# Performance work log

Measured on AMD Instinct MI355X. Metric: run time of the kernel, lower is better.

Reference implementation:

```python
import jax, jax.numpy as jnp
import numpy as np
import math

G, T, D, B = 20000, 1536, 512, 256
TOPK = 32


def setup_inputs() -> dict:
    key = jax.random.key(0)
    k1, k2, k3, k4 = jax.random.split(key, 4)
    tg_dec = jax.random.normal(k1, (G, D), dtype=jnp.float32)
    tf_base = jax.random.normal(k2, (T, D), dtype=jnp.float32)
    tf_expr = jax.random.normal(k3, (B, T), dtype=jnp.float32)
    motif_mask = jax.random.randint(k4, (G, T), 0, 2).astype(jnp.int32)
    scale = jnp.full((1,), 0.1, dtype=jnp.float32)  # nn.Parameter scale
    return {"tg_dec": tg_dec, "tf_base": tf_base, "tf_expr": tf_expr,
            "motif_mask": motif_mask, "scale": scale}


def reference(tg_dec, tf_base, tf_expr, motif_mask, scale):
    # scaled similarity: [G, T]
    sim = jnp.matmul(tg_dec, tf_base.T) / math.sqrt(tf_base.shape[1])
    # masked fill where motif prior is absent
    sim = jnp.where(motif_mask == 0, -jnp.inf, sim)
    attn = jax.nn.softmax(sim, axis=-1)
    attn = jnp.nan_to_num(attn, nan=0.0)
    # top-k selection + scatter mask + renormalize
    _, topk_idx = jax.lax.top_k(attn, TOPK)              # [G, TOPK]
    rows = jnp.arange(attn.shape[0])[:, None]
    mask = jnp.zeros_like(attn).at[rows, topk_idx].set(1.0)
    attn = attn * mask
    attn = attn / (attn.sum(axis=-1, keepdims=True) + 1e-8)
    # weighted combine: [B, G]
    tf_scalar = jnp.matmul(tf_expr, attn.T)
    # dropout is identity in eval mode
    return (scale[0] * tf_scalar, attn)
```

## Files before the change

kernel.cpp:

```cpp
#include <hip/hip_runtime.h>
#include <cstdint>

typedef unsigned short u16;
typedef unsigned int   u32;
typedef unsigned long long u64;

#define G_ROWS 20000
#define G_PAD  20096
#define T_DIM  1536
#define D_DIM  512
#define B_DIM  256
#define TOPK   32
#define SIM_SCALE 0.04419417382415922f
#define SQRT_D    22.62741699796952f
#define BOUND_EPS 2.0e-4f

typedef __bf16 bf16x8 __attribute__((ext_vector_type(8)));
typedef float  f32x4  __attribute__((ext_vector_type(4)));

__device__ __forceinline__ u16 f2bf(float f) {
  u32 u = __float_as_uint(f);
  u += 0x7fffu + ((u >> 16) & 1u);
  return (u16)(u >> 16);
}
__device__ __forceinline__ float bf2f(u16 h) {
  return __uint_as_float(((u32)h) << 16);
}
__device__ __forceinline__ u32 fkey(float v) {
  u32 b = __float_as_uint(v);
  return (b & 0x80000000u) ? ~b : (b | 0x80000000u);
}
__device__ __forceinline__ float funkey(u32 o) {
  u32 b = (o & 0x80000000u) ? (o & 0x7FFFFFFFu) : ~o;
  return __uint_as_float(b);
}

__global__ __launch_bounds__(256) void prep(const float* __restrict__ tg_dec,
                                            const float* __restrict__ tf_base,
                                            const float* __restrict__ tf_expr,
                                            u16* __restrict__ Ah, u16* __restrict__ Al,
                                            u16* __restrict__ Bh, u16* __restrict__ Bl,
                                            float* __restrict__ tfT)
{
  __shared__ float tile[32][33];
  const int b = blockIdx.x;
  const int tid = threadIdx.x;
  if (b < 10816) {
    const float* src; u16 *hi, *lo; int valid_rows; int bb;
    if (b < 10048) { src = tg_dec; hi = Ah; lo = Al; valid_rows = G_ROWS; bb = b; }
    else           { src = tf_base; hi = Bh; lo = Bl; valid_rows = T_DIM; bb = b - 10048; }
    size_t i = ((size_t)bb * 256 + tid) * 4;
    int row = (int)(i >> 9);
    float4 a = make_float4(0.f, 0.f, 0.f, 0.f);
    if (row < valid_rows) a = *(const float4*)(src + i);
    float v[4] = {a.x, a.y, a.z, a.w};
    u16 h[4], l[4];
#pragma unroll
    for (int c = 0; c < 4; ++c) {
      h[c] = f2bf(v[c]);
      l[c] = f2bf(v[c] - bf2f(h[c]));
    }
    *(uint2*)(hi + i) = make_uint2((u32)h[0] | ((u32)h[1] << 16), (u32)h[2] | ((u32)h[3] << 16));
    *(uint2*)(lo + i) = make_uint2((u32)l[0] | ((u32)l[1] << 16), (u32)l[2] | ((u32)l[3] << 16));
  } else {
    const int t = b - 10816;
    const int x = tid & 31, y = tid >> 5;
    const int bt = (t % 48) * 32;
    const int bb = (t / 48) * 32;
#pragma unroll
    for (int i = 0; i < 32; i += 8) tile[y + i][x] = tf_expr[(size_t)(bb + y + i) * T_DIM + bt + x];
    __syncthreads();
#pragma unroll
    for (int i = 0; i < 32; i += 8) tfT[(size_t)(bt + y + i) * B_DIM + bb + x] = tile[x][y + i];
  }
}

__device__ __forceinline__ void gl16(const u16* g, u16* l) {
  __builtin_amdgcn_global_load_lds((__attribute__((address_space(1))) void*)(void*)g,
                                   (__attribute__((address_space(3))) void*)l, 16, 0, 0);
}

#define NBX 6
#define NWG 474

__global__ __launch_bounds__(512, 2) void gemm_split(const u16* __restrict__ Ah, const u16* __restrict__ Al,
                                                     const u16* __restrict__ Bh, const u16* __restrict__ Bl,
                                                     const int* __restrict__ Mask,
                                                     float* __restrict__ Sim)
{
  __shared__ u16 sm[65536];

  const int orig = blockIdx.x;
  const int xcd  = orig & 7;
  const int q    = NWG >> 3, r = NWG & 7;
  const int wgid = (xcd < r ? xcd * (q + 1) : r * (q + 1) + (xcd - r) * q) + (orig >> 3);
  const int by   = wgid / NBX;
  const int bx   = wgid - by * NBX;
  const int bm0  = by * 256;
  const int bn0  = bx * 256;

  const int tid  = threadIdx.x;
  const int lane = tid & 63;
  const int wv   = tid >> 6;
  const int wm   = wv >> 2;
  const int wn   = wv & 3;
  const int la8  = lane << 3;

  const int sub  = wv << 1;
  const int srow = lane & 15;
  const int skc  = (lane >> 4) << 3;
  const u16* gA0  = Ah + (size_t)(bm0 + (sub + 0) * 16 + srow) * 512 + skc;
  const u16* gA1  = Ah + (size_t)(bm0 + (sub + 1) * 16 + srow) * 512 + skc;
  const u16* gAl0 = Al + (size_t)(bm0 + (sub + 0) * 16 + srow) * 512 + skc;
  const u16* gAl1 = Al + (size_t)(bm0 + (sub + 1) * 16 + srow) * 512 + skc;
  const u16* gB0  = Bh + (size_t)(bn0 + (sub + 0) * 16 + srow) * 512 + skc;
  const u16* gB1  = Bh + (size_t)(bn0 + (sub + 1) * 16 + srow) * 512 + skc;
  const u16* gBl0 = Bl + (size_t)(bn0 + (sub + 0) * 16 + srow) * 512 + skc;
  const u16* gBl1 = Bl + (size_t)(bn0 + (sub + 1) * 16 + srow) * 512 + skc;

#define STAGE_A(p, ktn) do {                                   \
    const size_t ko = (size_t)(ktn) << 5;                      \
    u16* d = sm + (p) * 16384 + sub * 512;                     \
    gl16(gA0 + ko,  d);                                        \
    gl16(gA1 + ko,  d + 512);                                  \
    gl16(gAl0 + ko, d + 8192);                                 \
    gl16(gAl1 + ko, d + 8192 + 512);                           \
  } while (0)
#define STAGE_B(p, ktn) do {                                   \
    const size_t ko = (size_t)(ktn) << 5;                      \
    u16* d = sm + 32768 + (p) * 16384 + sub * 512;             \
    gl16(gB0 + ko,  d);                                        \
    gl16(gB1 + ko,  d + 512);                                  \
    gl16(gBl0 + ko, d + 8192);                                 \
    gl16(gBl1 + ko, d + 8192 + 512);                           \
  } while (0)

  f32x4 acc[8][4];
#pragma unroll
  for (int i = 0; i < 8; ++i)
#pragma unroll
    for (int j = 0; j < 4; ++j) acc[i][j] = (f32x4){0.f, 0.f, 0.f, 0.f};

  bf16x8 aH[4], aL[4], bH[4], bL[4];

#define READ_A(rbA, half) do {                                                     \
    _Pragma("unroll")                                                              \
    for (int i = 0; i < 4; ++i) {                                                  \
      aH[i] = *(const bf16x8*)((rbA) + (wm * 8 + (half) * 4 + i) * 512 + la8);     \
      aL[i] = *(const bf16x8*)((rbA) + 8192 + (wm * 8 + (half) * 4 + i) * 512 + la8); \
    }                                                                              \
  } while (0)
#define READ_B(rbB, half) do {                                                     \
    _Pragma("unroll")                                                              \
    for (int i = 0; i < 2; ++i) {                                                  \
      bH[(half) * 2 + i] = *(const bf16x8*)((rbB) + (wn * 4 + (half) * 2 + i) * 512 + la8); \
      bL[(half) * 2 + i] = *(const bf16x8*)((rbB) + 8192 + (wn * 4 + (half) * 2 + i) * 512 + la8); \
    }                                                                              \
  } while (0)
#define MFMA_Q(qm, qn) do {                                                        \
    _Pragma("unroll")                                                              \
    for (int m2 = 0; m2 < 4; ++m2)                                                 \
      _Pragma("unroll")                                                            \
      for (int n2 = 0; n2 < 2; ++n2) {                                             \
        const int mi = (qm) * 4 + m2, ni = (qn) * 2 + n2;                          \
        acc[mi][ni] = __builtin_amdgcn_mfma_f32_16x16x32_bf16(aH[m2], bH[ni], acc[mi][ni], 0, 0, 0); \
        acc[mi][ni] = __builtin_amdgcn_mfma_f32_16x16x32_bf16(aH[m2], bL[ni], acc[mi][ni], 0, 0, 0); \
        acc[mi][ni] = __builtin_amdgcn_mfma_f32_16x16x32_bf16(aL[m2], bH[ni], acc[mi][ni], 0, 0, 0); \
      }                                                                            \
  } while (0)
#define SBAR do { __builtin_amdgcn_sched_barrier(0); __builtin_amdgcn_s_barrier(); __builtin_amdgcn_sched_barrier(0); } while (0)

  STAGE_A(0, 0);
  STAGE_B(0, 0);
  STAGE_A(1, 1);

#pragma unroll 2
  for (int kt = 0; kt < 16; ++kt) {
    const u16* rbA = sm + (kt & 1) * 16384;
    const u16* rbB = sm + 32768 + (kt & 1) * 16384;

    if (kt < 15) asm volatile("s_waitcnt vmcnt(4)" ::: "memory");
    else         asm volatile("s_waitcnt vmcnt(0)" ::: "memory");
    SBAR;

    READ_A(rbA, 0);
    READ_B(rbB, 0);
    if (kt < 15) STAGE_B((kt + 1) & 1, kt + 1);
    MFMA_Q(0, 0);
    READ_B(rbB, 1);
    MFMA_Q(0, 1);
    READ_A(rbA, 1);
    MFMA_Q(1, 0);

    SBAR;
    if (kt < 14) STAGE_A(kt & 1, kt + 2);
    __builtin_amdgcn_s_setprio(1);
    MFMA_Q(1, 1);
    __builtin_amdgcn_s_setprio(0);
  }
#undef STAGE_A
#undef STAGE_B
#undef READ_A
#undef READ_B
#undef MFMA_Q
#undef SBAR

  const float NEG_INF = __uint_as_float(0xff800000u);
  const int erow0 = bm0 + (wm << 7) + ((lane >> 4) << 2);
  const int ecol0 = bn0 + (wn << 6) + (lane & 15);
#pragma unroll
  for (int mi = 0; mi < 8; ++mi)
#pragma unroll
    for (int rr = 0; rr < 4; ++rr) {
      int row = erow0 + mi * 16 + rr;
      if (row < G_ROWS) {
        const int* mrow = Mask + (size_t)row * T_DIM + ecol0;
        float*     srow = Sim  + (size_t)row * T_DIM + ecol0;
#pragma unroll
        for (int ni = 0; ni < 4; ++ni) {
          int m = mrow[ni * 16];
          srow[ni * 16] = m ? acc[mi][ni][rr] * SIM_SCALE : NEG_INF;
        }
      }
    }
}

__device__ __forceinline__ int count_ge(const float* v, float tau) {
  int c = 0;
#pragma unroll
  for (int j = 0; j < 24; ++j) c += (int)__popcll(__ballot(v[j] >= tau));
  return c;
}
__device__ __forceinline__ u64 bitonic64_desc(u64 key, int lane) {
#pragma unroll
  for (int k = 2; k <= 64; k <<= 1) {
#pragma unroll
    for (int j = k >> 1; j > 0; j >>= 1) {
      u64 p = __shfl_xor(key, j, 64);
      bool lower = (lane & j) == 0;
      bool asc   = (lane & k) != 0;
      u64 mn = (key < p) ? key : p;
      u64 mx = (key < p) ? p : key;
      key = (lower == asc) ? mn : mx;
    }
  }
  return key;
}

__global__ __launch_bounds__(256) void topk_kernel(float* __restrict__ Sim,
                                                   const float* __restrict__ tg_dec,
                                                   const float* __restrict__ tf_base,
                                                   int* __restrict__ tIdx, float* __restrict__ tW)
{
  __shared__ u32 cval[4][64];
  __shared__ int cidxs[4][64];
  const int lane = threadIdx.x & 63;
  const int wv   = threadIdx.x >> 6;
  const int g    = blockIdx.x * 4 + wv;
  float* row = Sim + (size_t)g * T_DIM;

  float v[24];
#pragma unroll
  for (int j = 0; j < 6; ++j) {
    float4 q = *(const float4*)(row + j * 256 + lane * 4);
    v[j * 4 + 0] = q.x; v[j * 4 + 1] = q.y; v[j * 4 + 2] = q.z; v[j * 4 + 3] = q.w;
  }

  const float TH0 = 1.25f, TH1 = 1.40f, TH2 = 1.55f, TH3 = 1.70f, TH4 = 1.85f, TH5 = 2.00f;
  int n0 = 0, n1 = 0, n2 = 0, n3 = 0, n4 = 0, n5 = 0, nv = 0;
#pragma unroll
  for (int j = 0; j < 24; ++j) {
    float x = v[j];
    n0 += (x >= TH0); n1 += (x >= TH1); n2 += (x >= TH2);
    n3 += (x >= TH3); n4 += (x >= TH4); n5 += (x >= TH5);
    nv += (x != -INFINITY);
  }
  u64 p0 = (u64)(u32)n0 | ((u64)(u32)n1 << 16) | ((u64)(u32)n2 << 32) | ((u64)(u32)n3 << 48);
  u64 p1 = (u64)(u32)n4 | ((u64)(u32)n5 << 16) | ((u64)(u32)nv << 32);
#pragma unroll
  for (int off = 32; off > 0; off >>= 1) {
    p0 += __shfl_xor(p0, off, 64);
    p1 += __shfl_xor(p1, off, 64);
  }
  int c[6];
  c[0] = (int)(p0 & 0xFFFF); c[1] = (int)((p0 >> 16) & 0xFFFF);
  c[2] = (int)((p0 >> 32) & 0xFFFF); c[3] = (int)((p0 >> 48) & 0xFFFF);
  c[4] = (int)(p1 & 0xFFFF); c[5] = (int)((p1 >> 16) & 0xFFFF);
  const int cvalid = (int)((p1 >> 32) & 0xFFFF);

  float tau; int cnt;
  if (cvalid <= 64) { tau = -3.0e38f; cnt = cvalid; }
  else {
    int is = -1;
#pragma unroll
    for (int i = 0; i < 6; ++i) if (c[i] >= 33) is = i;
    const float THv[7] = {TH0, TH1, TH2, TH3, TH4, TH5, 8.0f};
    if (is >= 0 && c[is] <= 64) { tau = THv[is]; cnt = c[is]; }
    else {
      float lo, hi;
      if (is < 0) { lo = -4.0f; hi = TH0; }
      else        { lo = THv[is]; hi = THv[is + 1]; }
      tau = lo; cnt = 1000;
      for (int it = 0; it < 16; ++it) {
        float mid = 0.5f * (lo + hi);
        int cm = count_ge(v, mid);
        if (cm > 64)      lo = mid;
        else if (cm < 33) hi = mid;
        else { tau = mid; cnt = cm; break; }
      }
      if (cnt == 1000) tau = lo;
    }
  }

  int base = 0;
#pragma unroll
  for (int j = 0; j < 24; ++j) {
    bool pred = (v[j] >= tau);
    u64 bmc = __ballot(pred);
    int pos = base + (int)__popcll(bmc & ((1ull << lane) - 1ull));
    int idx = (j >> 2) * 256 + lane * 4 + (j & 3);
    if (pred && pos < 64) { cval[wv][pos] = fkey(v[j]); cidxs[wv][pos] = idx; }
    base += (int)__popcll(bmc);
  }
  const int cnt_eff = (base < 64) ? base : 64;

  u64 key = 0;
  if (lane < cnt_eff)
    key = ((u64)cval[wv][lane] << 32) | (u64)(u32)(~(u32)cidxs[wv][lane]);

  key = bitonic64_desc(key, lane);
  int   myidx = (int)(~(u32)key);
  float myv   = (key != 0) ? funkey((u32)(key >> 32)) : -INFINITY;

  float v31 = __shfl(myv, 31, 64);
  float v32 = __shfl(myv, 32, 64);
  if (cnt_eff > TOPK && (v31 - v32) < 2.0f * BOUND_EPS) {
    bool flag = (lane < cnt_eff) &&
                (myv >= v32 - 2.0f * BOUND_EPS) && (myv <= v31 + 2.0f * BOUND_EPS);
    if (flag) {
      const float* arow_g = tg_dec + (size_t)g * D_DIM;
      const float* brow   = tf_base + (size_t)myidx * D_DIM;
      float s1 = 0.f, s2 = 0.f;
#pragma unroll 8
      for (int k = 0; k < 384; k += 4) {
        float4 av = *(const float4*)(arow_g + k);
        float4 bv = *(const float4*)(brow + k);
        s1 = fmaf(av.x, bv.x, s1); s1 = fmaf(av.y, bv.y, s1);
        s1 = fmaf(av.z, bv.z, s1); s1 = fmaf(av.w, bv.w, s1);
      }
#pragma unroll 8
      for (int k = 384; k < 512; k += 4) {
        float4 av = *(const float4*)(arow_g + k);
        float4 bv = *(const float4*)(brow + k);
        s2 = fmaf(av.x, bv.x, s2); s2 = fmaf(av.y, bv.y, s2);
        s2 = fmaf(av.z, bv.z, s2); s2 = fmaf(av.w, bv.w, s2);
      }
      myv = (s1 + s2) / SQRT_D;
      key = ((u64)fkey(myv) << 32) | (u64)(u32)(~(u32)myidx);
    }
    key = bitonic64_desc(key, lane);
    myidx = (int)(~(u32)key);
    myv   = (key != 0) ? funkey((u32)(key >> 32)) : -INFINITY;
  }

  const bool selme = (lane < TOPK) && (lane < cnt_eff);
  float mx = __shfl(myv, 0, 64);
  float e = selme ? __expf(myv - mx) : 0.f;
  float E = e;
#pragma unroll
  for (int off = 32; off > 0; off >>= 1) E += __shfl_xor(E, off, 64);
  float rden = (E > 0.f) ? (1.f / E) : 0.f;
  float w = e * rden;

  const float4 z4 = make_float4(0.f, 0.f, 0.f, 0.f);
#pragma unroll
  for (int j = 0; j < 6; ++j) *(float4*)(row + j * 256 + lane * 4) = z4;
  asm volatile("s_waitcnt vmcnt(0)" ::: "memory");
  if (selme) row[myidx] = w;

  if (cnt_eff < TOPK && lane >= cnt_eff && lane < TOPK) {
    tIdx[(size_t)g * TOPK + lane] = 0; tW[(size_t)g * TOPK + lane] = 0.f;
  }
  if (selme) {
    tIdx[(size_t)g * TOPK + lane] = myidx;
    tW[(size_t)g * TOPK + lane]   = w;
  }
}

__global__ __launch_bounds__(256) void combine_kernel(const float* __restrict__ tfT, const int* __restrict__ tIdx,
                                                      const float* __restrict__ tW, const float* __restrict__ scalep,
                                                      float* __restrict__ out0)
{
  __shared__ int   sIdx[16 * 32];
  __shared__ float sW[16 * 32];
  const int tid  = threadIdx.x;
  const int lane = tid & 63;
  const int wv   = tid >> 6;
  const int g0   = blockIdx.x * 16;
  for (int i = tid; i < 512; i += 256) {
    sIdx[i] = tIdx[(size_t)g0 * 32 + i];
    sW[i]   = tW[(size_t)g0 * 32 + i];
  }
  __syncthreads();
  const float scale = scalep[0];
  const int gl = wv << 2;
  float acc[4][4];
#pragma unroll
  for (int gi = 0; gi < 4; ++gi)
#pragma unroll
    for (int c = 0; c < 4; ++c) acc[gi][c] = 0.f;

#pragma unroll 4
  for (int k = 0; k < 32; ++k) {
#pragma unroll
    for (int gi = 0; gi < 4; ++gi) {
      int   t = sIdx[(gl + gi) * 32 + k];
      float w = sW[(gl + gi) * 32 + k];
      float4 vv = *(const float4*)(tfT + (size_t)t * B_DIM + lane * 4);
      acc[gi][0] = fmaf(w, vv.x, acc[gi][0]);
      acc[gi][1] = fmaf(w, vv.y, acc[gi][1]);
      acc[gi][2] = fmaf(w, vv.z, acc[gi][2]);
      acc[gi][3] = fmaf(w, vv.w, acc[gi][3]);
    }
  }
#pragma unroll
  for (int c = 0; c < 4; ++c) {
    float4 o = make_float4(scale * acc[0][c], scale * acc[1][c], scale * acc[2][c], scale * acc[3][c]);
    *(float4*)(out0 + (size_t)(lane * 4 + c) * G_ROWS + g0 + gl) = o;
  }
}

extern "C" void kernel_launch(void* const* d_in, const int* in_sizes, int n_in,
                              void* d_out, int out_size, void* d_ws, size_t ws_size,
                              hipStream_t stream)
{
  const float* tg_dec     = (const float*)d_in[0];
  const float* tf_base    = (const float*)d_in[1];
  const float* tf_expr    = (const float*)d_in[2];
  const int*   motif_mask = (const int*)d_in[3];
  const float* scale      = (const float*)d_in[4];

  float* out0 = (float*)d_out;
  float* attn = out0 + (size_t)B_DIM * G_ROWS;

  char* ws = (char*)d_ws;
  u16*   Ah    = (u16*)(ws);
  u16*   Al    = (u16*)(ws + 20578304);
  u16*   Bh    = (u16*)(ws + 41156608);
  u16*   Bl    = (u16*)(ws + 42729472);
  float* tfT   = (float*)(ws + 44302336);
  int*   tIdx  = (int*)(ws + 45875200);
  float* tW    = (float*)(ws + 48435200);

  prep<<<11200, 256, 0, stream>>>(tg_dec, tf_base, tf_expr, Ah, Al, Bh, Bl, tfT);
  gemm_split<<<NWG, 512, 0, stream>>>(Ah, Al, Bh, Bl, motif_mask, attn);
  topk_kernel<<<5000, 256, 0, stream>>>(attn, tg_dec, tf_base, tIdx, tW);
  combine_kernel<<<1250, 256, 0, stream>>>(tfT, tIdx, tW, scale, out0);
}
```

Baseline: 440.8 us.

## Pack motif mask into bitmask in prep, apply in topk, restructure GEMM barriers

The int32 motif mask is packed into a 32-bit-per-32-column bitmask during prep and applied in the top-k kernel, so the GEMM epilogue no longer reads the full mask. The bitmask is stored in the output buffer region, which combine overwrites later. The GEMM main loop is split into four barrier-separated phases with explicit lgkmcnt waits, and setprio now wraps every MFMA quarter. Zeroing stores and output stores switch to nontemporal. The extra barriers may reduce overlap inside the GEMM loop.

Measured after the change: 456.6 us. 3.6% more time.

```diff
diff --git a/kernel.cpp b/kernel.cpp
--- a/kernel.cpp
+++ b/kernel.cpp
@@ -38,9 +38,11 @@
 __global__ __launch_bounds__(256) void prep(const float* __restrict__ tg_dec,
                                             const float* __restrict__ tf_base,
                                             const float* __restrict__ tf_expr,
+                                            const int* __restrict__ mask,
                                             u16* __restrict__ Ah, u16* __restrict__ Al,
                                             u16* __restrict__ Bh, u16* __restrict__ Bl,
-                                            float* __restrict__ tfT)
+                                            float* __restrict__ tfT,
+                                            u32* __restrict__ bits)
 {
   __shared__ float tile[32][33];
   const int b = blockIdx.x;
@@ -62,7 +64,7 @@
     }
     *(uint2*)(hi + i) = make_uint2((u32)h[0] | ((u32)h[1] << 16), (u32)h[2] | ((u32)h[3] << 16));
     *(uint2*)(lo + i) = make_uint2((u32)l[0] | ((u32)l[1] << 16), (u32)l[2] | ((u32)l[3] << 16));
-  } else {
+  } else if (b < 11200) {
     const int t = b - 10816;
     const int x = tid & 31, y = tid >> 5;
     const int bt = (t % 48) * 32;
@@ -72,6 +74,19 @@
     __syncthreads();
 #pragma unroll
     for (int i = 0; i < 32; i += 8) tfT[(size_t)(bt + y + i) * B_DIM + bb + x] = tile[x][y + i];
+  } else {
+    const int w = (b - 11200) * 256 + tid;
+    const int* mp = mask + (size_t)w * 32;
+    u32 bw = 0;
+#pragma unroll
+    for (int r = 0; r < 8; ++r) {
+      int4 m = *(const int4*)(mp + r * 4);
+      bw |= (m.x ? 1u : 0u) << (r * 4 + 0);
+      bw |= (m.y ? 1u : 0u) << (r * 4 + 1);
+      bw |= (m.z ? 1u : 0u) << (r * 4 + 2);
+      bw |= (m.w ? 1u : 0u) << (r * 4 + 3);
+    }
+    bits[w] = bw;
   }
 }
 
@@ -85,7 +100,6 @@
 
 __global__ __launch_bounds__(512, 2) void gemm_split(const u16* __restrict__ Ah, const u16* __restrict__ Al,
                                                      const u16* __restrict__ Bh, const u16* __restrict__ Bl,
-                                                     const int* __restrict__ Mask,
                                                      float* __restrict__ Sim)
 {
   __shared__ u16 sm[65536];
@@ -158,6 +172,7 @@
     }                                                                              \
   } while (0)
 #define MFMA_Q(qm, qn) do {                                                        \
+    __builtin_amdgcn_s_setprio(1);                                                 \
     _Pragma("unroll")                                                              \
     for (int m2 = 0; m2 < 4; ++m2)                                                 \
       _Pragma("unroll")                                                            \
@@ -167,8 +182,10 @@
         acc[mi][ni] = __builtin_amdgcn_mfma_f32_16x16x32_bf16(aH[m2], bL[ni], acc[mi][ni], 0, 0, 0); \
         acc[mi][ni] = __builtin_amdgcn_mfma_f32_16x16x32_bf16(aL[m2], bH[ni], acc[mi][ni], 0, 0, 0); \
       }                                                                            \
+    __builtin_amdgcn_s_setprio(0);                                                 \
   } while (0)
-#define SBAR do { __builtin_amdgcn_sched_barrier(0); __builtin_amdgcn_s_barrier(); __builtin_amdgcn_sched_barrier(0); } while (0)
+#define LGKM0 do { asm volatile("s_waitcnt lgkmcnt(0)" ::: "memory"); __builtin_amdgcn_sched_barrier(0); } while (0)
+#define BAR   do { __builtin_amdgcn_sched_barrier(0); __builtin_amdgcn_s_barrier(); } while (0)
 
   STAGE_A(0, 0);
   STAGE_B(0, 0);
@@ -181,31 +198,35 @@
 
     if (kt < 15) asm volatile("s_waitcnt vmcnt(4)" ::: "memory");
     else         asm volatile("s_waitcnt vmcnt(0)" ::: "memory");
-    SBAR;
-
+    BAR;
     READ_A(rbA, 0);
     READ_B(rbB, 0);
+    LGKM0;
+    MFMA_Q(0, 0);
+    BAR;
+
     if (kt < 15) STAGE_B((kt + 1) & 1, kt + 1);
-    MFMA_Q(0, 0);
     READ_B(rbB, 1);
+    LGKM0;
     MFMA_Q(0, 1);
+    BAR;
+
     READ_A(rbA, 1);
+    LGKM0;
     MFMA_Q(1, 0);
-
-    SBAR;
+    BAR;
+
     if (kt < 14) STAGE_A(kt & 1, kt + 2);
-    __builtin_amdgcn_s_setprio(1);
     MFMA_Q(1, 1);
-    __builtin_amdgcn_s_setprio(0);
   }
 #undef STAGE_A
 #undef STAGE_B
 #undef READ_A
 #undef READ_B
 #undef MFMA_Q
-#undef SBAR
-
-  const float NEG_INF = __uint_as_float(0xff800000u);
+#undef LGKM0
+#undef BAR
+
   const int erow0 = bm0 + (wm << 7) + ((lane >> 4) << 2);
   const int ecol0 = bn0 + (wn << 6) + (lane & 15);
 #pragma unroll
@@ -214,13 +235,9 @@
     for (int rr = 0; rr < 4; ++rr) {
       int row = erow0 + mi * 16 + rr;
       if (row < G_ROWS) {
-        const int* mrow = Mask + (size_t)row * T_DIM + ecol0;
-        float*     srow = Sim  + (size_t)row * T_DIM + ecol0;
-#pragma unroll
-        for (int ni = 0; ni < 4; ++ni) {
-          int m = mrow[ni * 16];
-          srow[ni * 16] = m ? acc[mi][ni][rr] * SIM_SCALE : NEG_INF;
-        }
+#pragma unroll
+        for (int ni = 0; ni < 4; ++ni)
+          Sim[(size_t)row * T_DIM + ecol0 + ni * 16] = acc[mi][ni][rr] * SIM_SCALE;
       }
     }
 }
@@ -247,7 +264,7 @@
   return key;
 }
 
-__global__ __launch_bounds__(256) void topk_kernel(float* __restrict__ Sim,
+__global__ __launch_bounds__(256) void topk_kernel(float* __restrict__ Sim, const u32* __restrict__ bits,
                                                    const float* __restrict__ tg_dec,
                                                    const float* __restrict__ tf_base,
                                                    int* __restrict__ tIdx, float* __restrict__ tW)
@@ -258,12 +275,17 @@
   const int wv   = threadIdx.x >> 6;
   const int g    = blockIdx.x * 4 + wv;
   float* row = Sim + (size_t)g * T_DIM;
+  const u32* brow = bits + (size_t)g * 48;
 
   float v[24];
 #pragma unroll
   for (int j = 0; j < 6; ++j) {
     float4 q = *(const float4*)(row + j * 256 + lane * 4);
-    v[j * 4 + 0] = q.x; v[j * 4 + 1] = q.y; v[j * 4 + 2] = q.z; v[j * 4 + 3] = q.w;
+    u32 nib = brow[8 * j + (lane >> 3)] >> ((lane & 7) << 2);
+    v[j * 4 + 0] = (nib & 1u) ? q.x : -INFINITY;
+    v[j * 4 + 1] = (nib & 2u) ? q.y : -INFINITY;
+    v[j * 4 + 2] = (nib & 4u) ? q.z : -INFINITY;
+    v[j * 4 + 3] = (nib & 8u) ? q.w : -INFINITY;
   }
 
   const float TH0 = 1.25f, TH1 = 1.40f, TH2 = 1.55f, TH3 = 1.70f, TH4 = 1.85f, TH5 = 2.00f;
@@ -339,19 +361,19 @@
                 (myv >= v32 - 2.0f * BOUND_EPS) && (myv <= v31 + 2.0f * BOUND_EPS);
     if (flag) {
       const float* arow_g = tg_dec + (size_t)g * D_DIM;
-      const float* brow   = tf_base + (size_t)myidx * D_DIM;
+      const float* brow2  = tf_base + (size_t)myidx * D_DIM;
       float s1 = 0.f, s2 = 0.f;
 #pragma unroll 8
       for (int k = 0; k < 384; k += 4) {
         float4 av = *(const float4*)(arow_g + k);
-        float4 bv = *(const float4*)(brow + k);
+        float4 bv = *(const float4*)(brow2 + k);
         s1 = fmaf(av.x, bv.x, s1); s1 = fmaf(av.y, bv.y, s1);
         s1 = fmaf(av.z, bv.z, s1); s1 = fmaf(av.w, bv.w, s1);
       }
 #pragma unroll 8
       for (int k = 384; k < 512; k += 4) {
         float4 av = *(const float4*)(arow_g + k);
-        float4 bv = *(const float4*)(brow + k);
+        float4 bv = *(const float4*)(brow2 + k);
         s2 = fmaf(av.x, bv.x, s2); s2 = fmaf(av.y, bv.y, s2);
         s2 = fmaf(av.z, bv.z, s2); s2 = fmaf(av.w, bv.w, s2);
       }
@@ -372,9 +394,10 @@
   float rden = (E > 0.f) ? (1.f / E) : 0.f;
   float w = e * rden;
 
-  const float4 z4 = make_float4(0.f, 0.f, 0.f, 0.f);
-#pragma unroll
-  for (int j = 0; j < 6; ++j) *(float4*)(row + j * 256 + lane * 4) = z4;
+  const f32x4 z4 = (f32x4){0.f, 0.f, 0.f, 0.f};
+#pragma unroll
+  for (int j = 0; j < 6; ++j)
+    __builtin_nontemporal_store(z4, (f32x4*)(row + j * 256 + lane * 4));
   asm volatile("s_waitcnt vmcnt(0)" ::: "memory");
   if (selme) row[myidx] = w;
 
@@ -425,8 +448,8 @@
   }
 #pragma unroll
   for (int c = 0; c < 4; ++c) {
-    float4 o = make_float4(scale * acc[0][c], scale * acc[1][c], scale * acc[2][c], scale * acc[3][c]);
-    *(float4*)(out0 + (size_t)(lane * 4 + c) * G_ROWS + g0 + gl) = o;
+    f32x4 o = (f32x4){scale * acc[0][c], scale * acc[1][c], scale * acc[2][c], scale * acc[3][c]};
+    __builtin_nontemporal_store(o, (f32x4*)(out0 + (size_t)(lane * 4 + c) * G_ROWS + g0 + gl));
   }
 }
 
@@ -442,6 +465,7 @@
 
   float* out0 = (float*)d_out;
   float* attn = out0 + (size_t)B_DIM * G_ROWS;
+  u32* bits = (u32*)d_out;
 
   char* ws = (char*)d_ws;
   u16*   Ah    = (u16*)(ws);
@@ -452,8 +476,8 @@
   int*   tIdx  = (int*)(ws + 45875200);
   float* tW    = (float*)(ws + 48435200);
 
-  prep<<<11200, 256, 0, stream>>>(tg_dec, tf_base, tf_expr, Ah, Al, Bh, Bl, tfT);
-  gemm_split<<<NWG, 512, 0, stream>>>(Ah, Al, Bh, Bl, motif_mask, attn);
-  topk_kernel<<<5000, 256, 0, stream>>>(attn, tg_dec, tf_base, tIdx, tW);
+  prep<<<14950, 256, 0, stream>>>(tg_dec, tf_base, tf_expr, motif_mask, Ah, Al, Bh, Bl, tfT, bits);
+  gemm_split<<<NWG, 512, 0, stream>>>(Ah, Al, Bh, Bl, attn);
+  topk_kernel<<<5000, 256, 0, stream>>>(attn, bits, tg_dec, tf_base, tIdx, tW);
   combine_kernel<<<1250, 256, 0, stream>>>(tfT, tIdx, tW, scale, out0);
 }
```
